# Kernel optimization log

Measured on AMD Instinct MI355X. Metric: run time of the kernel, lower is better.

Reference implementation:

```python
import jax, jax.numpy as jnp
import numpy as np

N_NODES = 50000
N_EDGES = 800000
DIM = 64
N_REL = 16
N_Q = 8192
FEAT = 4
N_LAYERS = 2


def setup_inputs() -> dict:
    key = jax.random.key(0)
    ks = jax.random.split(key, 16)
    s = 0.1
    return {
        "node_feat": jax.random.normal(ks[0], (N_NODES, FEAT), jnp.float32),
        "edge_index": jax.random.randint(ks[1], (2, N_EDGES), 0, N_NODES),
        "edge_type": jax.random.randint(ks[2], (N_EDGES,), 0, N_REL),
        "heads": jax.random.randint(ks[3], (N_Q,), 0, N_NODES),
        "rels": jax.random.randint(ks[4], (N_Q,), 0, N_REL),
        "tails": jax.random.randint(ks[5], (N_Q,), 0, N_NODES),
        # parameters (stored as [in, out] so y = x @ W + b)
        "in_w": jax.random.normal(ks[6], (FEAT, DIM), jnp.float32) * s,
        "in_b": jnp.zeros((DIM,), jnp.float32),
        "rel_w": jax.random.normal(ks[7], (N_LAYERS, N_REL, DIM, DIM), jnp.float32) * s,
        "self_w": jax.random.normal(ks[8], (N_LAYERS, DIM, DIM), jnp.float32) * s,
        "self_b": jnp.zeros((N_LAYERS, DIM), jnp.float32),
        "rel_emb": jax.random.normal(ks[9], (N_REL, DIM), jnp.float32) * s,
        "sc_w1": jax.random.normal(ks[10], (3 * DIM, DIM), jnp.float32) * s,
        "sc_b1": jnp.zeros((DIM,), jnp.float32),
        "sc_w2": jax.random.normal(ks[11], (DIM, 1), jnp.float32) * s,
        "sc_b2": jnp.zeros((1,), jnp.float32),
    }


def reference(node_feat, edge_index, edge_type, heads, rels, tails,
              in_w, in_b, rel_w, self_w, self_b, rel_emb,
              sc_w1, sc_b1, sc_w2, sc_b2):
    N = node_feat.shape[0]
    src, dst = edge_index[0], edge_index[1]
    # encoder input projection
    x = jax.nn.relu(node_feat @ in_w + in_b)  # [N, D]
    # degree normalization (same deg for every layer)
    deg = jax.ops.segment_sum(jnp.ones_like(dst, dtype=x.dtype), dst, num_segments=N)
    deg = jnp.maximum(deg, 1.0)[:, None]  # [N, 1]
    L = rel_w.shape[0]
    for l in range(L):
        out = x @ self_w[l] + self_b[l]  # self-loop, [N, D]
        # per-relation transform of every node, then per-edge gather by (src, rel)
        # equals the torch per-relation masked gather->matmul->scatter_add
        xw = jnp.einsum('nd,rdo->nro', x, rel_w[l])  # [N, R, D]
        msg = xw[src, edge_type]                     # [E, D]
        agg = jax.ops.segment_sum(msg, dst, num_segments=N)  # [N, D]
        x = jax.nn.relu(out + agg / deg)
    # scoring
    z_h = x[heads]
    z_t = x[tails]
    r = rel_emb[rels]
    c = jnp.concatenate([z_h, z_t, r], axis=-1)  # [Q, 3D]
    h = jax.nn.relu(c @ sc_w1 + sc_b1)
    return (h @ sc_w2 + sc_b2)[:, 0]  # [Q]
```

## Files before the change

kernel.cpp:

```cpp
#include <hip/hip_runtime.h>
#include <hip/hip_bf16.h>
#include <cstdint>
#include <cstddef>

#define N_NODES 50000
#define N_EDGES 800000
#define DIM 64
#define N_REL 16
#define N_Q 8192
#define NKEY (N_NODES * 16)
#define KDIM 1088
#define SROW 1096
#define TILE 32
#define NKB 34
#define WTL (4 * NKB * 512)
#define NBKT 196

#define NB_PROJ 12500
#define NB_WPREP 544
#define NB_BINA 196

typedef __attribute__((ext_vector_type(8))) short bf16x8;
typedef __attribute__((ext_vector_type(4))) float f32x4;

__device__ __forceinline__ float bcast_lane(float v, int l) {
    return __int_as_float(__builtin_amdgcn_readlane(__float_as_int(v), l));
}
__device__ __forceinline__ unsigned short f2bf(float f) {
    unsigned int b = __float_as_uint(f);
    return (unsigned short)((b + 0x7FFFu + ((b >> 16) & 1u)) >> 16);
}
__device__ __forceinline__ float bf2f(unsigned short u) {
    return __uint_as_float(((unsigned int)u) << 16);
}

__global__ __launch_bounds__(256) void k_prep(
    const float* __restrict__ nf, const float* __restrict__ inw,
    const float* __restrict__ inb, unsigned short* __restrict__ xbf,
    const float* __restrict__ rel_w, const float* __restrict__ self_w,
    unsigned short* __restrict__ wt, const int* __restrict__ dst,
    int* __restrict__ btot)
{
    __shared__ int h[NBKT];
    const int b = blockIdx.x, tid = threadIdx.x;
    if (b < NB_PROJ) {
        int t = b * 256 + tid;
        int n = t >> 6, o = t & 63;
        float4 f = *reinterpret_cast<const float4*>(nf + (size_t)n * 4);
        float a = inb[o] + f.x * inw[o] + f.y * inw[64 + o] + f.z * inw[128 + o] + f.w * inw[192 + o];
        xbf[t] = f2bf(a > 0.f ? a : 0.f);
    } else if (b < NB_PROJ + NB_WPREP) {
        int i = (b - NB_PROJ) * 256 + tid;
        int j = i & 7;
        int lane = (i >> 3) & 63;
        int rest = i >> 9;
        int t = rest % NKB;
        int gl = rest / NKB;
        int g = gl & 3;
        int l = gl >> 2;
        int col = g * 16 + (lane & 15);
        int k = t * 32 + (lane >> 4) * 8 + j;
        float v;
        if (k < 1024) {
            int r = k >> 6, d = k & 63;
            v = rel_w[(((size_t)l * 16 + r) * 64 + d) * 64 + col];
        } else {
            int d = k - 1024;
            v = self_w[((size_t)l * 64 + d) * 64 + col];
        }
        wt[i] = f2bf(v);
    } else {
        const int t = tid;
        if (t < NBKT) h[t] = 0;
        __syncthreads();
        const int e0 = (b - NB_PROJ - NB_WPREP) * 4096;
        #pragma unroll
        for (int j = 0; j < 16; ++j) {
            int e = e0 + j * 256 + t;
            if (e < N_EDGES) atomicAdd(&h[dst[e] >> 8], 1);
        }
        __syncthreads();
        if (t < NBKT && h[t]) atomicAdd(&btot[t], h[t]);
    }
}

__global__ __launch_bounds__(256) void k_binS(
    const int* __restrict__ btot, int* __restrict__ bbase, int* __restrict__ gcur)
{
    const int t = threadIdx.x;
    int v = (t < NBKT) ? btot[t] : 0;
    const int lane = t & 63, wid = t >> 6;
    int incl = v;
    #pragma unroll
    for (int o = 1; o < 64; o <<= 1) { int u = __shfl_up(incl, o); if (lane >= o) incl += u; }
    __shared__ int ws[4];
    if (lane == 63) ws[wid] = incl;
    __syncthreads();
    int wb = 0;
    #pragma unroll
    for (int w = 0; w < 4; ++w) if (w < wid) wb += ws[w];
    int excl = wb + incl - v;
    if (t < NBKT) { bbase[t] = excl; gcur[t] = excl; }
    if (t == NBKT - 1) bbase[NBKT] = excl + v;
}

__global__ __launch_bounds__(256) void k_binB(
    const int* __restrict__ src, const int* __restrict__ dst, const int* __restrict__ et,
    int* __restrict__ gcur, unsigned int* __restrict__ scratch)
{
    __shared__ int cnt[NBKT], base[NBKT], lcur[NBKT];
    const int t = threadIdx.x;
    if (t < NBKT) cnt[t] = 0;
    __syncthreads();
    const int e0 = blockIdx.x * 4096;
    int dv[16];
    #pragma unroll
    for (int j = 0; j < 16; ++j) {
        int e = e0 + j * 256 + t;
        dv[j] = (e < N_EDGES) ? dst[e] : -1;
        if (dv[j] >= 0) atomicAdd(&cnt[dv[j] >> 8], 1);
    }
    __syncthreads();
    if (t < NBKT) {
        base[t] = cnt[t] ? atomicAdd(&gcur[t], cnt[t]) : 0;
        lcur[t] = 0;
    }
    __syncthreads();
    #pragma unroll
    for (int j = 0; j < 16; ++j) {
        int e = e0 + j * 256 + t;
        if (dv[j] >= 0) {
            int b = dv[j] >> 8;
            int pos = base[b] + atomicAdd(&lcur[b], 1);
            unsigned p = ((unsigned)src[e] << 12) | ((unsigned)(dv[j] & 255) << 4) | (unsigned)et[e];
            scratch[pos] = p;
        }
    }
}

__global__ __launch_bounds__(1024) void k_key2(
    const int* __restrict__ bbase, const unsigned int* __restrict__ scratch,
    int* __restrict__ offs, unsigned int* __restrict__ csr)
{
    __shared__ int hist[4096];
    __shared__ int wsum[16];
    const int t = threadIdx.x;
    const int b = blockIdx.x;
    const int k0 = b * 4096;
    #pragma unroll
    for (int j = 0; j < 4; ++j) hist[t + j * 1024] = 0;
    __syncthreads();
    const int E0 = bbase[b], E1 = bbase[b + 1];
    for (int e = E0 + t; e < E1; e += 1024)
        atomicAdd(&hist[scratch[e] & 0xFFFu], 1);
    __syncthreads();
    int4 h4 = *reinterpret_cast<int4*>(&hist[t * 4]);
    int run = h4.x + h4.y + h4.z + h4.w;
    const int lane = t & 63, wid = t >> 6;
    int incl = run;
    #pragma unroll
    for (int o = 1; o < 64; o <<= 1) { int u = __shfl_up(incl, o); if (lane >= o) incl += u; }
    if (lane == 63) wsum[wid] = incl;
    __syncthreads();
    if (wid == 0) {
        int wv = (lane < 16) ? wsum[lane] : 0;
        #pragma unroll
        for (int o = 1; o < 16; o <<= 1) { int u = __shfl_up(wv, o); if (lane >= o) wv += u; }
        if (lane < 16) wsum[lane] = wv;
    }
    __syncthreads();
    int texcl = (wid ? wsum[wid - 1] : 0) + incl - run;
    int4 cur;
    cur.x = E0 + texcl;
    cur.y = cur.x + h4.x;
    cur.z = cur.y + h4.y;
    cur.w = cur.z + h4.z;
    *reinterpret_cast<int4*>(&hist[t * 4]) = cur;
    if (k0 + t * 4 < NKEY)
        *reinterpret_cast<int4*>(&offs[k0 + t * 4]) = cur;
    if (b == NBKT - 1 && t == 0) offs[NKEY] = N_EDGES;
    __syncthreads();
    for (int e = E0 + t; e < E1; e += 1024) {
        unsigned p = scratch[e];
        int pos = atomicAdd(&hist[p & 0xFFFu], 1);
        csr[pos] = ((p >> 12) << 7) | (p & 15u);
    }
}

__global__ __launch_bounds__(1024, 8) void k_layer(
    const unsigned short* __restrict__ xbf_in,
    const int* __restrict__ offs,
    const unsigned int* __restrict__ csr,
    const unsigned short* __restrict__ wt,
    const float* __restrict__ selfb,
    unsigned short* __restrict__ xbf_out)
{
    alignas(16) __shared__ unsigned short S[TILE * SROW];
    const int tid = threadIdx.x, lane = tid & 63;
    const int wid = __builtin_amdgcn_readfirstlane(tid >> 6);
    const int nb = blockIdx.x * TILE;

    #pragma unroll
    for (int s = 0; s < 2; ++s) {
        unsigned int* Sr = reinterpret_cast<unsigned int*>(&S[(wid * 2 + s) * SROW]);
        #pragma unroll
        for (int i = 0; i < 8; ++i) Sr[lane + i * 64] = 0u;
        if (lane < 32) Sr[512 + lane] = 0u;
    }

    #pragma unroll 1
    for (int s = 0; s < 2; ++s) {
        const int nl = wid * 2 + s;
        const int node = nb + nl;
        if (node >= N_NODES) break;
        const int A = offs[node * 16];
        const int B = offs[node * 16 + 16];
        S[nl * SROW + 1024 + lane] = xbf_in[(size_t)node * 64 + lane];
        const int deg = B - A;
        if (deg <= 0) continue;
        const float inv = 1.0f / (float)(deg > 1 ? deg : 1);

        const unsigned loff = (unsigned)(lane << 1);
        unsigned c0[8], c1[8];
        float x0[8], x1[8];
        int cur = -1;
        float acc = 0.f;

        auto loadb = [&](unsigned (&cv)[8], float (&xv)[8], int eb) {
            #pragma unroll
            for (int j = 0; j < 8; ++j) {
                int idx = eb + j;
                idx = idx < B - 1 ? idx : B - 1;
                cv[j] = csr[idx];
            }
            #pragma unroll
            for (int j = 0; j < 8; ++j) {
                unsigned off = (cv[j] & 0xFFFFFF80u) | loff;
                xv[j] = bf2f(*reinterpret_cast<const unsigned short*>(
                    reinterpret_cast<const char*>(xbf_in) + off));
            }
        };
        auto accum = [&](unsigned (&cv)[8], float (&xv)[8], int m) {
            #pragma unroll
            for (int j = 0; j < 8; ++j) {
                if (j < m) {
                    int rj = (int)(cv[j] & 15u);
                    if (rj != cur) {
                        if (cur >= 0) S[nl * SROW + cur * 64 + lane] = f2bf(acc * inv);
                        cur = rj;
                        acc = 0.f;
                    }
                    acc += xv[j];
                }
            }
        };

        int e0 = A;
        int m0 = deg > 8 ? 8 : deg;
        loadb(c0, x0, e0);
        for (;;) {
            int e1 = e0 + 8;
            int m1 = B - e1;
            m1 = m1 > 8 ? 8 : m1;
            if (m1 > 0) loadb(c1, x1, e1);
            accum(c0, x0, m0);
            if (m1 <= 0) break;
            int e2 = e1 + 8;
            m0 = B - e2;
            m0 = m0 > 8 ? 8 : m0;
            if (m0 > 0) loadb(c0, x0, e2);
            accum(c1, x1, m1);
            if (m0 <= 0) break;
            e0 = e2;
        }
        if (cur >= 0) S[nl * SROW + cur * 64 + lane] = f2bf(acc * inv);
    }
    __syncthreads();

    const int g = wid & 3, kq = wid >> 2;
    const int t0 = kq * 8 + (kq < 2 ? kq : 2);
    const int tn = kq < 2 ? 9 : 8;
    const int colg = lane & 15, kg = lane >> 4;
    f32x4 acc0 = {0.f, 0.f, 0.f, 0.f};
    f32x4 acc1 = {0.f, 0.f, 0.f, 0.f};
    const unsigned short* wb = wt + (size_t)g * (NKB * 512) + (size_t)lane * 8 + (size_t)t0 * 512;
    const unsigned short* sa0 = &S[colg * SROW + kg * 8 + t0 * 32];
    const unsigned short* sa1 = &S[(16 + colg) * SROW + kg * 8 + t0 * 32];
    #pragma unroll 1
    for (int t = 0; t < tn; ++t) {
        bf16x8 b  = *reinterpret_cast<const bf16x8*>(wb + (size_t)t * 512);
        bf16x8 a0 = *reinterpret_cast<const bf16x8*>(sa0 + t * 32);
        bf16x8 a1 = *reinterpret_cast<const bf16x8*>(sa1 + t * 32);
        acc0 = __builtin_amdgcn_mfma_f32_16x16x32_bf16(a0, b, acc0, 0, 0, 0);
        acc1 = __builtin_amdgcn_mfma_f32_16x16x32_bf16(a1, b, acc1, 0, 0, 0);
    }
    __syncthreads();
    float4* scr = reinterpret_cast<float4*>(S);
    if (kq > 0) {
        int base = ((kq - 1) * 4 + g) * 128 + lane;
        scr[base]      = make_float4(acc0[0], acc0[1], acc0[2], acc0[3]);
        scr[base + 64] = make_float4(acc1[0], acc1[1], acc1[2], acc1[3]);
    }
    __syncthreads();
    if (kq == 0) {
        #pragma unroll
        for (int p = 0; p < 3; ++p) {
            int base = (p * 4 + g) * 128 + lane;
            float4 q0 = scr[base], q1 = scr[base + 64];
            acc0[0] += q0.x; acc0[1] += q0.y; acc0[2] += q0.z; acc0[3] += q0.w;
            acc1[0] += q1.x; acc1[1] += q1.y; acc1[2] += q1.z; acc1[3] += q1.w;
        }
        const int col = g * 16 + colg;
        const float sb = selfb[col];
        #pragma unroll
        for (int j = 0; j < 4; ++j) {
            int n0 = nb + kg * 4 + j;
            float v0 = acc0[j] + sb;
            v0 = v0 > 0.f ? v0 : 0.f;
            if (n0 < N_NODES) xbf_out[(size_t)n0 * 64 + col] = f2bf(v0);
            int n1 = nb + 16 + kg * 4 + j;
            float v1 = acc1[j] + sb;
            v1 = v1 > 0.f ? v1 : 0.f;
            if (n1 < N_NODES) xbf_out[(size_t)n1 * 64 + col] = f2bf(v1);
        }
    }
}

__global__ __launch_bounds__(256) void k_score(
    const unsigned short* __restrict__ x, const int* __restrict__ heads,
    const int* __restrict__ rels, const int* __restrict__ tails,
    const float* __restrict__ rel_emb, const float* __restrict__ w1,
    const float* __restrict__ b1, const float* __restrict__ w2,
    const float* __restrict__ b2, float* __restrict__ out)
{
    int q = blockIdx.x * 4 + (threadIdx.x >> 6);
    if (q >= N_Q) return;
    int lane = threadIdx.x & 63;
    float zh = bf2f(x[(size_t)heads[q] * 64 + lane]);
    float zt = bf2f(x[(size_t)tails[q] * 64 + lane]);
    float re = rel_emb[(size_t)rels[q] * 64 + lane];
    float acc = b1[lane];
    #pragma unroll 8
    for (int k = 0; k < 64; ++k)
        acc += bcast_lane(zh, k) * w1[k * 64 + lane];
    #pragma unroll 8
    for (int k = 0; k < 64; ++k)
        acc += bcast_lane(zt, k) * w1[(64 + k) * 64 + lane];
    #pragma unroll 8
    for (int k = 0; k < 64; ++k)
        acc += bcast_lane(re, k) * w1[(128 + k) * 64 + lane];
    float h = acc > 0.f ? acc : 0.f;
    float p = h * w2[lane];
    #pragma unroll
    for (int off = 32; off > 0; off >>= 1) p += __shfl_xor(p, off);
    if (lane == 0) out[q] = p + b2[0];
}

extern "C" void kernel_launch(void* const* d_in, const int* in_sizes, int n_in,
                              void* d_out, int out_size, void* d_ws, size_t ws_size,
                              hipStream_t stream)
{
    const float* node_feat = (const float*)d_in[0];
    const int* edge_index  = (const int*)d_in[1];
    const int* edge_type   = (const int*)d_in[2];
    const int* heads       = (const int*)d_in[3];
    const int* rels        = (const int*)d_in[4];
    const int* tails       = (const int*)d_in[5];
    const float* in_w      = (const float*)d_in[6];
    const float* in_b      = (const float*)d_in[7];
    const float* rel_w     = (const float*)d_in[8];
    const float* self_w    = (const float*)d_in[9];
    const float* self_b    = (const float*)d_in[10];
    const float* rel_emb   = (const float*)d_in[11];
    const float* sc_w1     = (const float*)d_in[12];
    const float* sc_b1     = (const float*)d_in[13];
    const float* sc_w2     = (const float*)d_in[14];
    const float* sc_b2     = (const float*)d_in[15];
    float* out = (float*)d_out;

    char* ws = (char*)d_ws;
    size_t off = 0;
    auto alloc = [&](size_t bytes) -> void* {
        void* p = ws + off;
        off = (off + bytes + 255) & ~(size_t)255;
        return p;
    };
    unsigned short* xbf_a = (unsigned short*)alloc((size_t)N_NODES * 64 * 2);
    unsigned short* xbf_b = (unsigned short*)alloc((size_t)N_NODES * 64 * 2);
    int* offs             = (int*)alloc((size_t)(NKEY + 1) * 4);
    unsigned int* scratch = (unsigned int*)alloc((size_t)N_EDGES * 4);
    unsigned int* csr     = (unsigned int*)alloc((size_t)N_EDGES * 4);
    unsigned short* wt    = (unsigned short*)alloc((size_t)2 * WTL * 2);
    int* btot             = (int*)alloc(NBKT * 4);
    int* bbase            = (int*)alloc((NBKT + 1) * 4);
    int* gcur             = (int*)alloc(NBKT * 4);

    const int* src = edge_index;
    const int* dst = edge_index + N_EDGES;

    hipMemsetAsync(btot, 0, NBKT * 4, stream);
    k_prep<<<NB_PROJ + NB_WPREP + NB_BINA, 256, 0, stream>>>(
        node_feat, in_w, in_b, xbf_a, rel_w, self_w, wt, dst, btot);
    k_binS<<<1, 256, 0, stream>>>(btot, bbase, gcur);
    k_binB<<<(N_EDGES + 4095) / 4096, 256, 0, stream>>>(src, dst, edge_type, gcur, scratch);
    k_key2<<<NBKT, 1024, 0, stream>>>(bbase, scratch, offs, csr);

    for (int l = 0; l < 2; ++l) {
        const unsigned short* xin = (l == 0) ? xbf_a : xbf_b;
        unsigned short* xout = (l == 0) ? xbf_b : xbf_a;
        k_layer<<<(N_NODES + TILE - 1) / TILE, 1024, 0, stream>>>(
            xin, offs, csr, wt + (size_t)l * WTL, self_b + l * 64, xout);
    }
    k_score<<<(N_Q + 3) / 4, 256, 0, stream>>>(xbf_a, heads, rels, tails, rel_emb,
                                               sc_w1, sc_b1, sc_w2, sc_b2, out);
}
```

Baseline: 162.7 us.

## Halve layer tile to 16 nodes and move scoring MLP onto MFMA

The layer kernel now processes 16 nodes per 512-thread block instead of 32 per 1024 threads. The K reduction is split across two wave groups of 17 k-blocks each, which shrinks the LDS tile and the cross-wave reduction and drops the tail bounds checks, since N_NODES divides by 16. The scoring kernel is rewritten to run the first MLP layer with bf16 MFMA over 16 queries per block, using sc_w1 and rel_emb pre-packed to bf16 in the prep kernel. This replaces the per-lane readlane FMA loops, at the cost of bf16 rounding on sc_w1 and rel_emb.

```diff
diff --git a/kernel.cpp b/kernel.cpp
--- a/kernel.cpp
+++ b/kernel.cpp
@@ -11,7 +11,7 @@
 #define NKEY (N_NODES * 16)
 #define KDIM 1088
 #define SROW 1096
-#define TILE 32
+#define TILE 16
 #define NKB 34
 #define WTL (4 * NKB * 512)
 #define NBKT 196
@@ -19,13 +19,12 @@
 #define NB_PROJ 12500
 #define NB_WPREP 544
 #define NB_BINA 196
+#define NB_W1P 48
+#define NB_REB 4
 
 typedef __attribute__((ext_vector_type(8))) short bf16x8;
 typedef __attribute__((ext_vector_type(4))) float f32x4;
 
-__device__ __forceinline__ float bcast_lane(float v, int l) {
-    return __int_as_float(__builtin_amdgcn_readlane(__float_as_int(v), l));
-}
 __device__ __forceinline__ unsigned short f2bf(float f) {
     unsigned int b = __float_as_uint(f);
     return (unsigned short)((b + 0x7FFFu + ((b >> 16) & 1u)) >> 16);
@@ -39,7 +38,9 @@
     const float* __restrict__ inb, unsigned short* __restrict__ xbf,
     const float* __restrict__ rel_w, const float* __restrict__ self_w,
     unsigned short* __restrict__ wt, const int* __restrict__ dst,
-    int* __restrict__ btot)
+    int* __restrict__ btot, const float* __restrict__ sc_w1,
+    unsigned short* __restrict__ w1p, const float* __restrict__ rel_emb,
+    unsigned short* __restrict__ reb)
 {
     __shared__ int h[NBKT];
     const int b = blockIdx.x, tid = threadIdx.x;
@@ -69,7 +70,7 @@
             v = self_w[((size_t)l * 64 + d) * 64 + col];
         }
         wt[i] = f2bf(v);
-    } else {
+    } else if (b < NB_PROJ + NB_WPREP + NB_BINA) {
         const int t = tid;
         if (t < NBKT) h[t] = 0;
         __syncthreads();
@@ -81,6 +82,19 @@
         }
         __syncthreads();
         if (t < NBKT && h[t]) atomicAdd(&btot[t], h[t]);
+    } else if (b < NB_PROJ + NB_WPREP + NB_BINA + NB_W1P) {
+        int i = (b - NB_PROJ - NB_WPREP - NB_BINA) * 256 + tid;
+        int j = i & 7;
+        int lane = (i >> 3) & 63;
+        int rest = i >> 9;
+        int t = rest % 6;
+        int g = rest / 6;
+        int col = g * 16 + (lane & 15);
+        int k = t * 32 + (lane >> 4) * 8 + j;
+        w1p[i] = f2bf(sc_w1[k * 64 + col]);
+    } else {
+        int i = (b - NB_PROJ - NB_WPREP - NB_BINA - NB_W1P) * 256 + tid;
+        if (i < N_REL * 64) reb[i] = f2bf(rel_emb[i]);
     }
 }
 
@@ -187,7 +201,7 @@
     }
 }
 
-__global__ __launch_bounds__(1024, 8) void k_layer(
+__global__ __launch_bounds__(512, 8) void k_layer(
     const unsigned short* __restrict__ xbf_in,
     const int* __restrict__ offs,
     const unsigned int* __restrict__ csr,
@@ -212,7 +226,6 @@
     for (int s = 0; s < 2; ++s) {
         const int nl = wid * 2 + s;
         const int node = nb + nl;
-        if (node >= N_NODES) break;
         const int A = offs[node * 16];
         const int B = offs[node * 16 + 16];
         S[nl * SROW + 1024 + lane] = xbf_in[(size_t)node * 64 + lane];
@@ -277,39 +290,27 @@
     }
     __syncthreads();
 
-    const int g = wid & 3, kq = wid >> 2;
-    const int t0 = kq * 8 + (kq < 2 ? kq : 2);
-    const int tn = kq < 2 ? 9 : 8;
+    const int g = wid & 3, kh = wid >> 2;
+    const int t0 = kh * 17;
     const int colg = lane & 15, kg = lane >> 4;
     f32x4 acc0 = {0.f, 0.f, 0.f, 0.f};
-    f32x4 acc1 = {0.f, 0.f, 0.f, 0.f};
     const unsigned short* wb = wt + (size_t)g * (NKB * 512) + (size_t)lane * 8 + (size_t)t0 * 512;
     const unsigned short* sa0 = &S[colg * SROW + kg * 8 + t0 * 32];
-    const unsigned short* sa1 = &S[(16 + colg) * SROW + kg * 8 + t0 * 32];
     #pragma unroll 1
-    for (int t = 0; t < tn; ++t) {
+    for (int t = 0; t < 17; ++t) {
         bf16x8 b  = *reinterpret_cast<const bf16x8*>(wb + (size_t)t * 512);
         bf16x8 a0 = *reinterpret_cast<const bf16x8*>(sa0 + t * 32);
-        bf16x8 a1 = *reinterpret_cast<const bf16x8*>(sa1 + t * 32);
         acc0 = __builtin_amdgcn_mfma_f32_16x16x32_bf16(a0, b, acc0, 0, 0, 0);
-        acc1 = __builtin_amdgcn_mfma_f32_16x16x32_bf16(a1, b, acc1, 0, 0, 0);
     }
     __syncthreads();
     float4* scr = reinterpret_cast<float4*>(S);
-    if (kq > 0) {
-        int base = ((kq - 1) * 4 + g) * 128 + lane;
-        scr[base]      = make_float4(acc0[0], acc0[1], acc0[2], acc0[3]);
-        scr[base + 64] = make_float4(acc1[0], acc1[1], acc1[2], acc1[3]);
-    }
-    __syncthreads();
-    if (kq == 0) {
-        #pragma unroll
-        for (int p = 0; p < 3; ++p) {
-            int base = (p * 4 + g) * 128 + lane;
-            float4 q0 = scr[base], q1 = scr[base + 64];
-            acc0[0] += q0.x; acc0[1] += q0.y; acc0[2] += q0.z; acc0[3] += q0.w;
-            acc1[0] += q1.x; acc1[1] += q1.y; acc1[2] += q1.z; acc1[3] += q1.w;
-        }
+    if (kh == 1) {
+        scr[g * 64 + lane] = make_float4(acc0[0], acc0[1], acc0[2], acc0[3]);
+    }
+    __syncthreads();
+    if (kh == 0) {
+        float4 q0 = scr[g * 64 + lane];
+        acc0[0] += q0.x; acc0[1] += q0.y; acc0[2] += q0.z; acc0[3] += q0.w;
         const int col = g * 16 + colg;
         const float sb = selfb[col];
         #pragma unroll
@@ -317,11 +318,7 @@
             int n0 = nb + kg * 4 + j;
             float v0 = acc0[j] + sb;
             v0 = v0 > 0.f ? v0 : 0.f;
-            if (n0 < N_NODES) xbf_out[(size_t)n0 * 64 + col] = f2bf(v0);
-            int n1 = nb + 16 + kg * 4 + j;
-            float v1 = acc1[j] + sb;
-            v1 = v1 > 0.f ? v1 : 0.f;
-            if (n1 < N_NODES) xbf_out[(size_t)n1 * 64 + col] = f2bf(v1);
+            xbf_out[(size_t)n0 * 64 + col] = f2bf(v0);
         }
     }
 }
@@ -329,31 +326,55 @@
 __global__ __launch_bounds__(256) void k_score(
     const unsigned short* __restrict__ x, const int* __restrict__ heads,
     const int* __restrict__ rels, const int* __restrict__ tails,
-    const float* __restrict__ rel_emb, const float* __restrict__ w1,
+    const unsigned short* __restrict__ reb, const unsigned short* __restrict__ w1p,
     const float* __restrict__ b1, const float* __restrict__ w2,
     const float* __restrict__ b2, float* __restrict__ out)
 {
-    int q = blockIdx.x * 4 + (threadIdx.x >> 6);
-    if (q >= N_Q) return;
-    int lane = threadIdx.x & 63;
-    float zh = bf2f(x[(size_t)heads[q] * 64 + lane]);
-    float zt = bf2f(x[(size_t)tails[q] * 64 + lane]);
-    float re = rel_emb[(size_t)rels[q] * 64 + lane];
-    float acc = b1[lane];
-    #pragma unroll 8
-    for (int k = 0; k < 64; ++k)
-        acc += bcast_lane(zh, k) * w1[k * 64 + lane];
-    #pragma unroll 8
-    for (int k = 0; k < 64; ++k)
-        acc += bcast_lane(zt, k) * w1[(64 + k) * 64 + lane];
-    #pragma unroll 8
-    for (int k = 0; k < 64; ++k)
-        acc += bcast_lane(re, k) * w1[(128 + k) * 64 + lane];
-    float h = acc > 0.f ? acc : 0.f;
-    float p = h * w2[lane];
-    #pragma unroll
-    for (int off = 32; off > 0; off >>= 1) p += __shfl_xor(p, off);
-    if (lane == 0) out[q] = p + b2[0];
+    __shared__ float scr[64];
+    const int tid = threadIdx.x, lane = tid & 63, w = tid >> 6;
+    const int qbase = blockIdx.x * 16;
+    const int ql = lane & 15, kg = lane >> 4;
+    const int q = qbase + ql;
+    const unsigned short* zh = x + (size_t)heads[q] * 64 + kg * 8;
+    const unsigned short* zt = x + (size_t)tails[q] * 64 + kg * 8;
+    const unsigned short* re = reb + rels[q] * 64 + kg * 8;
+    bf16x8 a0 = *reinterpret_cast<const bf16x8*>(zh);
+    bf16x8 a1 = *reinterpret_cast<const bf16x8*>(zh + 32);
+    bf16x8 a2 = *reinterpret_cast<const bf16x8*>(zt);
+    bf16x8 a3 = *reinterpret_cast<const bf16x8*>(zt + 32);
+    bf16x8 a4 = *reinterpret_cast<const bf16x8*>(re);
+    bf16x8 a5 = *reinterpret_cast<const bf16x8*>(re + 32);
+    const unsigned short* wb = w1p + (size_t)w * (6 * 512) + (size_t)lane * 8;
+    f32x4 acc = {0.f, 0.f, 0.f, 0.f};
+    acc = __builtin_amdgcn_mfma_f32_16x16x32_bf16(a0, *reinterpret_cast<const bf16x8*>(wb + 0 * 512), acc, 0, 0, 0);
+    acc = __builtin_amdgcn_mfma_f32_16x16x32_bf16(a1, *reinterpret_cast<const bf16x8*>(wb + 1 * 512), acc, 0, 0, 0);
+    acc = __builtin_amdgcn_mfma_f32_16x16x32_bf16(a2, *reinterpret_cast<const bf16x8*>(wb + 2 * 512), acc, 0, 0, 0);
+    acc = __builtin_amdgcn_mfma_f32_16x16x32_bf16(a3, *reinterpret_cast<const bf16x8*>(wb + 3 * 512), acc, 0, 0, 0);
+    acc = __builtin_amdgcn_mfma_f32_16x16x32_bf16(a4, *reinterpret_cast<const bf16x8*>(wb + 4 * 512), acc, 0, 0, 0);
+    acc = __builtin_amdgcn_mfma_f32_16x16x32_bf16(a5, *reinterpret_cast<const bf16x8*>(wb + 5 * 512), acc, 0, 0, 0);
+    const int col = w * 16 + ql;
+    const float b1c = b1[col], w2c = w2[col];
+    float p[4];
+    #pragma unroll
+    for (int j = 0; j < 4; ++j) {
+        float hh = acc[j] + b1c;
+        hh = hh > 0.f ? hh : 0.f;
+        p[j] = hh * w2c;
+    }
+    #pragma unroll
+    for (int o = 1; o < 16; o <<= 1) {
+        p[0] += __shfl_xor(p[0], o);
+        p[1] += __shfl_xor(p[1], o);
+        p[2] += __shfl_xor(p[2], o);
+        p[3] += __shfl_xor(p[3], o);
+    }
+    if (ql == 0) {
+        #pragma unroll
+        for (int j = 0; j < 4; ++j) scr[w * 16 + kg * 4 + j] = p[j];
+    }
+    __syncthreads();
+    if (tid < 16)
+        out[qbase + tid] = scr[tid] + scr[16 + tid] + scr[32 + tid] + scr[48 + tid] + b2[0];
 }
 
 extern "C" void kernel_launch(void* const* d_in, const int* in_sizes, int n_in,
@@ -391,6 +412,8 @@
     unsigned int* scratch = (unsigned int*)alloc((size_t)N_EDGES * 4);
     unsigned int* csr     = (unsigned int*)alloc((size_t)N_EDGES * 4);
     unsigned short* wt    = (unsigned short*)alloc((size_t)2 * WTL * 2);
+    unsigned short* w1p   = (unsigned short*)alloc((size_t)4 * 6 * 512 * 2);
+    unsigned short* reb   = (unsigned short*)alloc((size_t)N_REL * 64 * 2);
     int* btot             = (int*)alloc(NBKT * 4);
     int* bbase            = (int*)alloc((NBKT + 1) * 4);
     int* gcur             = (int*)alloc(NBKT * 4);
@@ -399,8 +422,9 @@
     const int* dst = edge_index + N_EDGES;
 
     hipMemsetAsync(btot, 0, NBKT * 4, stream);
-    k_prep<<<NB_PROJ + NB_WPREP + NB_BINA, 256, 0, stream>>>(
-        node_feat, in_w, in_b, xbf_a, rel_w, self_w, wt, dst, btot);
+    k_prep<<<NB_PROJ + NB_WPREP + NB_BINA + NB_W1P + NB_REB, 256, 0, stream>>>(
+        node_feat, in_w, in_b, xbf_a, rel_w, self_w, wt, dst, btot,
+        sc_w1, w1p, rel_emb, reb);
     k_binS<<<1, 256, 0, stream>>>(btot, bbase, gcur);
     k_binB<<<(N_EDGES + 4095) / 4096, 256, 0, stream>>>(src, dst, edge_type, gcur, scratch);
     k_key2<<<NBKT, 1024, 0, stream>>>(bbase, scratch, offs, csr);
@@ -408,9 +432,9 @@
     for (int l = 0; l < 2; ++l) {
         const unsigned short* xin = (l == 0) ? xbf_a : xbf_b;
         unsigned short* xout = (l == 0) ? xbf_b : xbf_a;
-        k_layer<<<(N_NODES + TILE - 1) / TILE, 1024, 0, stream>>>(
+        k_layer<<<N_NODES / TILE, 512, 0, stream>>>(
             xin, offs, csr, wt + (size_t)l * WTL, self_b + l * 64, xout);
     }
-    k_score<<<(N_Q + 3) / 4, 256, 0, stream>>>(xbf_a, heads, rels, tails, rel_emb,
-                                               sc_w1, sc_b1, sc_w2, sc_b2, out);
-}
+    k_score<<<N_Q / 16, 256, 0, stream>>>(xbf_a, heads, rels, tails, reb, w1p,
+                                          sc_b1, sc_w2, sc_b2, out);
+}
```

Result: faster. 141.7 us (-13.0%).
